# Performance work log

Measured on AMD Instinct MI355X. Metric: run time of the kernel, lower is better.

Reference implementation:

```python
import jax, jax.numpy as jnp
import numpy as np

K = 32
TEMPERATURE = 0.1
RTOL, ATOL = 1e-5, 1e-5


def _embed(x, W1, b1, W2, b2, W3, b3):
    h = jax.nn.gelu(x @ W1.T + b1, approximate=False)
    h = jax.nn.gelu(h @ W2.T + b2, approximate=False)
    return jax.nn.sigmoid(h @ W3.T + b3)


def setup_inputs() -> dict:
    key = jax.random.key(0)
    ks = jax.random.split(key, 9)
    Q, N, D_IN, D_E = 256, 16384, 256, 64
    s = lambda fan_in: 1.0 / np.sqrt(fan_in)
    return {
        "x": jax.random.normal(ks[0], (Q, D_IN), jnp.float32),
        "support_x": jax.random.normal(ks[1], (N, D_IN), jnp.float32),
        "support_labels": jax.random.uniform(ks[2], (N, 1), jnp.float32),
        "W1": jax.random.normal(ks[3], (D_E, D_IN), jnp.float32) * s(D_IN),
        "b1": jax.random.normal(ks[4], (D_E,), jnp.float32) * s(D_IN),
        "W2": jax.random.normal(ks[5], (D_E, D_E), jnp.float32) * s(D_E),
        "b2": jax.random.normal(ks[6], (D_E,), jnp.float32) * s(D_E),
        "W3": jax.random.normal(ks[7], (D_E, D_E), jnp.float32) * s(D_E),
        "b3": jax.random.normal(ks[8], (D_E,), jnp.float32) * s(D_E),
    }


def reference(x, support_x, support_labels, W1, b1, W2, b2, W3, b3):
    # query embeddings [Q, D]; support embeddings [N, D] (set_support is no_grad)
    q = _embed(x, W1, b1, W2, b2, W3, b3)
    s = jax.lax.stop_gradient(_embed(support_x, W1, b1, W2, b2, W3, b3))
    # torch.cdist p=2 via expanded squared distances
    d2 = (jnp.sum(q * q, -1)[:, None] + jnp.sum(s * s, -1)[None, :]
          - 2.0 * (q @ s.T))
    dist = jnp.sqrt(jnp.maximum(d2, 0.0))  # [Q, N]
    # isclose mask: |q - s| <= atol + rtol*|s|, all over feature dim
    close = jnp.abs(q[:, None, :] - s[None, :, :]) <= (ATOL + RTOL * jnp.abs(s)[None, :, :])
    mask = jnp.all(close, axis=-1)  # [Q, N]
    dist = jnp.where(mask, jnp.inf, dist)
    # top-k smallest distances
    neg_top, idx = jax.lax.top_k(-dist, K)  # [Q, K]
    topd = -neg_top
    neighbor_labels = support_labels[idx].squeeze(-1)  # [Q, K]
    weights = jax.nn.softmax(-topd / TEMPERATURE, axis=1)
    return jnp.sum(weights * neighbor_labels, axis=1)  # [Q]
```

## Files before the change

kernel.cpp:

```cpp
#include <hip/hip_runtime.h>
#include <math.h>

#define D_IN   256
#define D_E    64
#define N_SUP  16384
#define NQ     256
#define KSEL   32
#define RTOLC  1e-5f
#define ATOLC  1e-5f
#define INV_T  10.0f

#define CHUNK  1024
#define NCH    16
#define QG     8
#define NQG    32

typedef unsigned long long ull;

__device__ __forceinline__ float gelu_exact(float x) {
    return 0.5f * x * (1.0f + erff(x * 0.70710678118654752440f));
}

__global__ __launch_bounds__(256) void prep_w(
    const float* __restrict__ W1, const float* __restrict__ W2,
    const float* __restrict__ W3,
    float* __restrict__ W1T, float* __restrict__ W2T, float* __restrict__ W3T)
{
    const int t = blockIdx.x * 256 + threadIdx.x;
    const int stride = gridDim.x * 256;
    for (int o = t; o < D_E * D_IN; o += stride) {
        int f = o >> 8, k = o & 255;
        W1T[k * D_E + f] = W1[o];
    }
    for (int o = t; o < D_E * D_E; o += stride) {
        int f = o >> 6, k = o & 63;
        W2T[k * D_E + f] = W2[o];
        W3T[k * D_E + f] = W3[o];
    }
}

__global__ __launch_bounds__(512, 6) void embed_kernel(
    const float* __restrict__ sx, const float* __restrict__ x,
    const float* __restrict__ W1T, const float* __restrict__ b1,
    const float* __restrict__ W2T, const float* __restrict__ b2,
    const float* __restrict__ W3T, const float* __restrict__ b3,
    float* __restrict__ s_emb, float* __restrict__ s_norm,
    float* __restrict__ q_emb, float* __restrict__ q_norm)
{
    __shared__ float xc[64][65];
    __shared__ float hA[64][65];
    __shared__ float hB[64][65];
    __shared__ float nsum[64][9];

    const int tid  = threadIdx.x;
    const int lane = tid & 63;
    const int wv   = tid >> 6;
    const int f0   = __builtin_amdgcn_readfirstlane(wv * 8);
    const bool isq = blockIdx.x >= (N_SUP / 64);
    const float* src = isq ? (x + (size_t)(blockIdx.x - N_SUP / 64) * 64 * D_IN)
                           : (sx + (size_t)blockIdx.x * 64 * D_IN);

    float acc[8];
    #pragma unroll
    for (int i = 0; i < 8; ++i) acc[i] = b1[f0 + i];

    for (int kc = 0; kc < 4; ++kc) {
        __syncthreads();
        #pragma unroll
        for (int i = 0; i < 2; ++i) {
            int g   = i * 512 + tid;
            int row = g >> 4;
            int c4  = g & 15;
            float4 v = *reinterpret_cast<const float4*>(
                src + (size_t)row * D_IN + kc * 64 + c4 * 4);
            xc[c4 * 4 + 0][row] = v.x; xc[c4 * 4 + 1][row] = v.y;
            xc[c4 * 4 + 2][row] = v.z; xc[c4 * 4 + 3][row] = v.w;
        }
        __syncthreads();
        const float* wbase = W1T + (size_t)(kc * 64) * D_E + f0;
        #pragma unroll 8
        for (int k = 0; k < 64; ++k) {
            float xk = xc[k][lane];
            const float* wk = wbase + k * D_E;
            #pragma unroll
            for (int f = 0; f < 8; ++f) acc[f] = fmaf(wk[f], xk, acc[f]);
        }
    }
    #pragma unroll
    for (int i = 0; i < 8; ++i) hA[f0 + i][lane] = gelu_exact(acc[i]);
    __syncthreads();

    float a2[8];
    #pragma unroll
    for (int i = 0; i < 8; ++i) a2[i] = b2[f0 + i];
    #pragma unroll 8
    for (int k = 0; k < D_E; ++k) {
        float hk = hA[k][lane];
        const float* wk = W2T + k * D_E + f0;
        #pragma unroll
        for (int f = 0; f < 8; ++f) a2[f] = fmaf(wk[f], hk, a2[f]);
    }
    #pragma unroll
    for (int i = 0; i < 8; ++i) hB[f0 + i][lane] = gelu_exact(a2[i]);
    __syncthreads();

    float a3[8];
    #pragma unroll
    for (int i = 0; i < 8; ++i) a3[i] = b3[f0 + i];
    #pragma unroll 8
    for (int k = 0; k < D_E; ++k) {
        float hk = hB[k][lane];
        const float* wk = W3T + k * D_E + f0;
        #pragma unroll
        for (int f = 0; f < 8; ++f) a3[f] = fmaf(wk[f], hk, a3[f]);
    }
    float e[8];
    float np = 0.0f;
    #pragma unroll
    for (int i = 0; i < 8; ++i) {
        e[i] = 1.0f / (1.0f + expf(-a3[i]));
        np = fmaf(e[i], e[i], np);
    }

    const int rowl = isq ? (blockIdx.x - N_SUP / 64) * 64 + lane
                         : blockIdx.x * 64 + lane;
    float* E   = isq ? q_emb  : s_emb;
    float* Nrm = isq ? q_norm : s_norm;
    float* erow = E + (size_t)rowl * D_E + f0;
    *reinterpret_cast<float4*>(erow)     = make_float4(e[0], e[1], e[2], e[3]);
    *reinterpret_cast<float4*>(erow + 4) = make_float4(e[4], e[5], e[6], e[7]);

    nsum[lane][wv] = np;
    __syncthreads();
    if (wv == 0) {
        float s = 0.0f;
        #pragma unroll
        for (int w = 0; w < 8; ++w) s += nsum[lane][w];
        Nrm[rowl] = s;
    }
}

__global__ __launch_bounds__(512, 4) void knn_phaseA(
    const float* __restrict__ s_emb, const float* __restrict__ s_norm,
    const float* __restrict__ q_emb, const float* __restrict__ q_norm,
    const float* __restrict__ labels, ull* __restrict__ cand)
{
    __shared__ float tile[64 * 68];
    __shared__ float d2l[QG][CHUNK];
    __shared__ ull   win_l[QG][KSEL];

    const int tid  = threadIdx.x;
    const int lane = tid & 63;
    const int wid  = tid >> 6;
    const int qg   = blockIdx.x >> 4;
    const int sc   = blockIdx.x & 15;
    const int qiu  = __builtin_amdgcn_readfirstlane(qg * QG + wid);

    const float* q0 = q_emb + (size_t)qiu * D_E;
    const float  qn = q_norm[qiu];

    for (int s = 0; s < 16; ++s) {
        __syncthreads();
        #pragma unroll
        for (int i = 0; i < 2; ++i) {
            int g   = i * 512 + tid;
            int row = g >> 4, c4 = g & 15;
            float4 v = *reinterpret_cast<const float4*>(
                s_emb + (size_t)(sc * CHUNK + s * 64 + row) * D_E + c4 * 4);
            *reinterpret_cast<float4*>(&tile[row * 68 + c4 * 4]) = v;
        }
        __syncthreads();

        const float* tr = &tile[lane * 68];
        float a = 0.0f;
        #pragma unroll
        for (int c = 0; c < 16; ++c) {
            float4 sv = *reinterpret_cast<const float4*>(tr + c * 4);
            a = fmaf(q0[c * 4 + 0], sv.x, a);
            a = fmaf(q0[c * 4 + 1], sv.y, a);
            a = fmaf(q0[c * 4 + 2], sv.z, a);
            a = fmaf(q0[c * 4 + 3], sv.w, a);
        }
        const int grow = sc * CHUNK + s * 64 + lane;
        float d2 = fmaxf(qn + s_norm[grow] - 2.0f * a, 0.0f);
        if (d2 < 1e-3f) {
            bool close = true;
            for (int k = 0; k < D_E; ++k) {
                float sv = tr[k];
                close = close && (fabsf(q0[k] - sv) <= (ATOLC + RTOLC * fabsf(sv)));
            }
            if (close) d2 = INFINITY;
        }
        d2l[wid][s * 64 + lane] = d2;
    }

    ull sk[16];
    #pragma unroll
    for (int j = 0; j < 16; ++j) {
        float d2 = d2l[wid][j * 64 + lane];
        sk[j] = ((ull)__float_as_uint(d2) << 10) | (unsigned)(j * 64 + lane);
    }

    #pragma unroll
    for (int k = 2; k <= 16; k <<= 1) {
        #pragma unroll
        for (int j = k >> 1; j > 0; j >>= 1) {
            #pragma unroll
            for (int i = 0; i < 16; ++i) {
                int ixj = i ^ j;
                if (ixj > i) {
                    if ((i & k) == 0) {
                        ull a_ = sk[i], b_ = sk[ixj];
                        bool c_ = b_ < a_;
                        sk[i] = c_ ? b_ : a_; sk[ixj] = c_ ? a_ : b_;
                    } else {
                        ull a_ = sk[i], b_ = sk[ixj];
                        bool c_ = a_ < b_;
                        sk[i] = c_ ? b_ : a_; sk[ixj] = c_ ? a_ : b_;
                    }
                }
            }
        }
    }

    ull lkey = sk[0];
    for (int it = 0; it < KSEL; ++it) {
        ull m = lkey;
        #pragma unroll
        for (int off = 1; off < 64; off <<= 1) {
            ull o = __shfl_xor(m, off);
            m = o < m ? o : m;
        }
        if (lane == it) win_l[wid][it] = m;
        if (lkey == m) {
            #pragma unroll
            for (int j = 0; j < 15; ++j) sk[j] = sk[j + 1];
            sk[15] = ~0ull;
            lkey = sk[0];
        }
    }

    if (lane < KSEL) {
        ull m = win_l[wid][lane];
        unsigned gidx = (unsigned)(sc * CHUNK) + (unsigned)(m & 1023u);
        float lab = labels[gidx];
        ull* dst = cand + ((size_t)qiu * NCH + sc) * KSEL;
        dst[lane] = ((ull)(unsigned)(m >> 10) << 32) | (ull)__float_as_uint(lab);
    }
}

__global__ __launch_bounds__(256) void knn_phaseB(
    const ull* __restrict__ cand, float* __restrict__ out)
{
    const int lane = threadIdx.x & 63;
    const int wid  = threadIdx.x >> 6;
    const int q    = blockIdx.x * 4 + wid;

    const bool act = lane < NCH;
    const ull* lst = cand + ((size_t)q * NCH + (lane & 15)) * KSEL;
    int ptr = 0;
    ull cur = act ? lst[0] : ~0ull;

    float d0 = 0.0f, sw = 0.0f, sl = 0.0f;
    for (int it = 0; it < KSEL; ++it) {
        unsigned mv = (unsigned)(cur >> 32);
        unsigned ml = (unsigned)cur;
        #pragma unroll
        for (int off = 1; off < 16; off <<= 1) {
            unsigned ov = __shfl_xor(mv, off);
            unsigned ol = __shfl_xor(ml, off);
            bool take = (ov < mv) || (ov == mv && (lane & off));
            mv = take ? ov : mv;
            ml = take ? ol : ml;
        }
        ull b = __ballot(act && (unsigned)(cur >> 32) == mv);
        int wl = (int)(__ffsll((long long)b) - 1);
        if (lane == wl) {
            ++ptr;
            cur = (ptr < KSEL) ? lst[ptr] : ~0ull;
        }
        if (lane == 0) {
            float d = sqrtf(__uint_as_float(mv));
            if (it == 0) d0 = d;
            float w = expf((d0 - d) * INV_T);
            sw += w;
            sl += w * __uint_as_float(ml);
        }
    }
    if (lane == 0) out[q] = sl / sw;
}

extern "C" void kernel_launch(void* const* d_in, const int* in_sizes, int n_in,
                              void* d_out, int out_size, void* d_ws, size_t ws_size,
                              hipStream_t stream) {
    const float* x      = (const float*)d_in[0];
    const float* sx     = (const float*)d_in[1];
    const float* labels = (const float*)d_in[2];
    const float* W1     = (const float*)d_in[3];
    const float* b1     = (const float*)d_in[4];
    const float* W2     = (const float*)d_in[5];
    const float* b2     = (const float*)d_in[6];
    const float* W3     = (const float*)d_in[7];
    const float* b3     = (const float*)d_in[8];
    float* out = (float*)d_out;

    float* ws     = (float*)d_ws;
    float* s_emb  = ws;
    float* s_norm = s_emb + N_SUP * D_E;
    float* q_emb  = s_norm + N_SUP;
    float* q_norm = q_emb + NQ * D_E;
    float* W1T    = q_norm + NQ;
    float* W2T    = W1T + D_IN * D_E;
    float* W3T    = W2T + D_E * D_E;
    ull*   cand   = (ull*)(W3T + D_E * D_E);

    prep_w<<<32, 256, 0, stream>>>(W1, W2, W3, W1T, W2T, W3T);
    embed_kernel<<<(N_SUP + NQ) / 64, 512, 0, stream>>>(
        sx, x, W1T, b1, W2T, b2, W3T, b3, s_emb, s_norm, q_emb, q_norm);
    knn_phaseA<<<NQG * NCH, 512, 0, stream>>>(s_emb, s_norm, q_emb, q_norm,
                                              labels, cand);
    knn_phaseB<<<NQ / 4, 256, 0, stream>>>(cand, out);
}
```

Before: 101.6 us.

## Restructure embed and kNN kernels with shared-memory weight tiles and double buffering

The embed kernel drops the separate weight-transpose kernel and now stages W1/W2/W3 through shared memory in double-buffered tiles, using 16-row blocks with 256 threads where each thread computes 4 features. The kNN phase A caches query embeddings in LDS, double-buffers support tiles, and remaps lanes so each wave covers 8 queries by 8 rows. Its top-k merge now reduces 32-bit distance keys with a ballot-based tie-break in place of 64-bit shuffles. These changes target global weight reads, one kernel launch, and shuffle cost, at the price of more blocks and lower declared occupancy in phase A.

New measurement: 111.5 us. +9.7%, slower.

```diff
diff --git a/kernel.cpp b/kernel.cpp
--- a/kernel.cpp
+++ b/kernel.cpp
@@ -14,6 +14,7 @@
 #define NCH    16
 #define QG     8
 #define NQG    32
+#define EROWS  16
 
 typedef unsigned long long ull;
 
@@ -21,132 +22,148 @@
     return 0.5f * x * (1.0f + erff(x * 0.70710678118654752440f));
 }
 
-__global__ __launch_bounds__(256) void prep_w(
-    const float* __restrict__ W1, const float* __restrict__ W2,
-    const float* __restrict__ W3,
-    float* __restrict__ W1T, float* __restrict__ W2T, float* __restrict__ W3T)
-{
-    const int t = blockIdx.x * 256 + threadIdx.x;
-    const int stride = gridDim.x * 256;
-    for (int o = t; o < D_E * D_IN; o += stride) {
-        int f = o >> 8, k = o & 255;
-        W1T[k * D_E + f] = W1[o];
-    }
-    for (int o = t; o < D_E * D_E; o += stride) {
-        int f = o >> 6, k = o & 63;
-        W2T[k * D_E + f] = W2[o];
-        W3T[k * D_E + f] = W3[o];
-    }
-}
-
-__global__ __launch_bounds__(512, 6) void embed_kernel(
+__global__ __launch_bounds__(256, 4) void embed_kernel(
     const float* __restrict__ sx, const float* __restrict__ x,
-    const float* __restrict__ W1T, const float* __restrict__ b1,
-    const float* __restrict__ W2T, const float* __restrict__ b2,
-    const float* __restrict__ W3T, const float* __restrict__ b3,
+    const float* __restrict__ W1, const float* __restrict__ b1,
+    const float* __restrict__ W2, const float* __restrict__ b2,
+    const float* __restrict__ W3, const float* __restrict__ b3,
     float* __restrict__ s_emb, float* __restrict__ s_norm,
     float* __restrict__ q_emb, float* __restrict__ q_norm)
 {
-    __shared__ float xc[64][65];
-    __shared__ float hA[64][65];
-    __shared__ float hB[64][65];
-    __shared__ float nsum[64][9];
-
-    const int tid  = threadIdx.x;
-    const int lane = tid & 63;
-    const int wv   = tid >> 6;
-    const int f0   = __builtin_amdgcn_readfirstlane(wv * 8);
-    const bool isq = blockIdx.x >= (N_SUP / 64);
-    const float* src = isq ? (x + (size_t)(blockIdx.x - N_SUP / 64) * 64 * D_IN)
-                           : (sx + (size_t)blockIdx.x * 64 * D_IN);
-
-    float acc[8];
-    #pragma unroll
-    for (int i = 0; i < 8; ++i) acc[i] = b1[f0 + i];
-
+    __shared__ float xc[2][64][17];
+    __shared__ float wc[2][64][68];
+    __shared__ float hA[64][17];
+    __shared__ float nsq[16][17];
+
+    const int tid = threadIdx.x;
+    const int r   = tid & 15;
+    const int fg4 = (tid >> 4) * 4;
+    const bool isq = blockIdx.x >= (N_SUP / EROWS);
+    const float* src = isq ? (x + (size_t)(blockIdx.x - N_SUP / EROWS) * EROWS * D_IN)
+                           : (sx + (size_t)blockIdx.x * EROWS * D_IN);
+
+    #define STAGE_X(kc_, b_)                                                   \
+        {                                                                      \
+            int row_ = tid >> 4, c4_ = tid & 15;                               \
+            float4 v_ = *reinterpret_cast<const float4*>(                      \
+                src + (size_t)row_ * D_IN + (kc_) * 64 + c4_ * 4);             \
+            xc[b_][c4_ * 4 + 0][row_] = v_.x;                                  \
+            xc[b_][c4_ * 4 + 1][row_] = v_.y;                                  \
+            xc[b_][c4_ * 4 + 2][row_] = v_.z;                                  \
+            xc[b_][c4_ * 4 + 3][row_] = v_.w;                                  \
+        }
+    #define STAGE_W1(kc_, b_)                                                  \
+        {                                                                      \
+            _Pragma("unroll")                                                  \
+            for (int i_ = 0; i_ < 4; ++i_) {                                   \
+                int g_ = i_ * 256 + tid;                                       \
+                int f_ = g_ >> 4, c4_ = g_ & 15;                               \
+                float4 w_ = *reinterpret_cast<const float4*>(                  \
+                    W1 + (size_t)f_ * D_IN + (kc_) * 64 + c4_ * 4);            \
+                wc[b_][c4_ * 4 + 0][f_] = w_.x;                                \
+                wc[b_][c4_ * 4 + 1][f_] = w_.y;                                \
+                wc[b_][c4_ * 4 + 2][f_] = w_.z;                                \
+                wc[b_][c4_ * 4 + 3][f_] = w_.w;                                \
+            }                                                                  \
+        }
+
+    STAGE_X(0, 0);
+    STAGE_W1(0, 0);
+    __syncthreads();
+
+    float4 bv1 = *reinterpret_cast<const float4*>(b1 + fg4);
+    float acc[4] = {bv1.x, bv1.y, bv1.z, bv1.w};
     for (int kc = 0; kc < 4; ++kc) {
-        __syncthreads();
-        #pragma unroll
-        for (int i = 0; i < 2; ++i) {
-            int g   = i * 512 + tid;
-            int row = g >> 4;
-            int c4  = g & 15;
-            float4 v = *reinterpret_cast<const float4*>(
-                src + (size_t)row * D_IN + kc * 64 + c4 * 4);
-            xc[c4 * 4 + 0][row] = v.x; xc[c4 * 4 + 1][row] = v.y;
-            xc[c4 * 4 + 2][row] = v.z; xc[c4 * 4 + 3][row] = v.w;
-        }
-        __syncthreads();
-        const float* wbase = W1T + (size_t)(kc * 64) * D_E + f0;
+        const int b = kc & 1;
+        if (kc < 3) { STAGE_X(kc + 1, b ^ 1); STAGE_W1(kc + 1, b ^ 1); }
         #pragma unroll 8
         for (int k = 0; k < 64; ++k) {
-            float xk = xc[k][lane];
-            const float* wk = wbase + k * D_E;
-            #pragma unroll
-            for (int f = 0; f < 8; ++f) acc[f] = fmaf(wk[f], xk, acc[f]);
-        }
-    }
-    #pragma unroll
-    for (int i = 0; i < 8; ++i) hA[f0 + i][lane] = gelu_exact(acc[i]);
-    __syncthreads();
-
-    float a2[8];
-    #pragma unroll
-    for (int i = 0; i < 8; ++i) a2[i] = b2[f0 + i];
+            float xk = xc[b][k][r];
+            float4 wv = *reinterpret_cast<const float4*>(&wc[b][k][fg4]);
+            acc[0] = fmaf(wv.x, xk, acc[0]);
+            acc[1] = fmaf(wv.y, xk, acc[1]);
+            acc[2] = fmaf(wv.z, xk, acc[2]);
+            acc[3] = fmaf(wv.w, xk, acc[3]);
+        }
+        __syncthreads();
+    }
+    #pragma unroll
+    for (int i = 0; i < 4; ++i) hA[fg4 + i][r] = gelu_exact(acc[i]);
+    #pragma unroll
+    for (int i = 0; i < 4; ++i) {
+        int g = i * 256 + tid;
+        int f = g >> 4, c4 = g & 15;
+        float4 w2 = *reinterpret_cast<const float4*>(W2 + (size_t)f * D_E + c4 * 4);
+        wc[0][c4 * 4 + 0][f] = w2.x; wc[0][c4 * 4 + 1][f] = w2.y;
+        wc[0][c4 * 4 + 2][f] = w2.z; wc[0][c4 * 4 + 3][f] = w2.w;
+        float4 w3 = *reinterpret_cast<const float4*>(W3 + (size_t)f * D_E + c4 * 4);
+        wc[1][c4 * 4 + 0][f] = w3.x; wc[1][c4 * 4 + 1][f] = w3.y;
+        wc[1][c4 * 4 + 2][f] = w3.z; wc[1][c4 * 4 + 3][f] = w3.w;
+    }
+    __syncthreads();
+
+    float4 bv2 = *reinterpret_cast<const float4*>(b2 + fg4);
+    float a2[4] = {bv2.x, bv2.y, bv2.z, bv2.w};
     #pragma unroll 8
     for (int k = 0; k < D_E; ++k) {
-        float hk = hA[k][lane];
-        const float* wk = W2T + k * D_E + f0;
-        #pragma unroll
-        for (int f = 0; f < 8; ++f) a2[f] = fmaf(wk[f], hk, a2[f]);
-    }
-    #pragma unroll
-    for (int i = 0; i < 8; ++i) hB[f0 + i][lane] = gelu_exact(a2[i]);
-    __syncthreads();
-
-    float a3[8];
-    #pragma unroll
-    for (int i = 0; i < 8; ++i) a3[i] = b3[f0 + i];
+        float hk = hA[k][r];
+        float4 wv = *reinterpret_cast<const float4*>(&wc[0][k][fg4]);
+        a2[0] = fmaf(wv.x, hk, a2[0]);
+        a2[1] = fmaf(wv.y, hk, a2[1]);
+        a2[2] = fmaf(wv.z, hk, a2[2]);
+        a2[3] = fmaf(wv.w, hk, a2[3]);
+    }
+    #pragma unroll
+    for (int i = 0; i < 4; ++i) xc[0][fg4 + i][r] = gelu_exact(a2[i]);
+    __syncthreads();
+
+    float4 bv3 = *reinterpret_cast<const float4*>(b3 + fg4);
+    float a3[4] = {bv3.x, bv3.y, bv3.z, bv3.w};
     #pragma unroll 8
     for (int k = 0; k < D_E; ++k) {
-        float hk = hB[k][lane];
-        const float* wk = W3T + k * D_E + f0;
-        #pragma unroll
-        for (int f = 0; f < 8; ++f) a3[f] = fmaf(wk[f], hk, a3[f]);
-    }
-    float e[8];
+        float hk = xc[0][k][r];
+        float4 wv = *reinterpret_cast<const float4*>(&wc[1][k][fg4]);
+        a3[0] = fmaf(wv.x, hk, a3[0]);
+        a3[1] = fmaf(wv.y, hk, a3[1]);
+        a3[2] = fmaf(wv.z, hk, a3[2]);
+        a3[3] = fmaf(wv.w, hk, a3[3]);
+    }
+    float e[4];
     float np = 0.0f;
     #pragma unroll
-    for (int i = 0; i < 8; ++i) {
+    for (int i = 0; i < 4; ++i) {
         e[i] = 1.0f / (1.0f + expf(-a3[i]));
         np = fmaf(e[i], e[i], np);
     }
 
-    const int rowl = isq ? (blockIdx.x - N_SUP / 64) * 64 + lane
-                         : blockIdx.x * 64 + lane;
+    const int rowg = (isq ? (blockIdx.x - N_SUP / EROWS) * EROWS : blockIdx.x * EROWS) + r;
     float* E   = isq ? q_emb  : s_emb;
     float* Nrm = isq ? q_norm : s_norm;
-    float* erow = E + (size_t)rowl * D_E + f0;
-    *reinterpret_cast<float4*>(erow)     = make_float4(e[0], e[1], e[2], e[3]);
-    *reinterpret_cast<float4*>(erow + 4) = make_float4(e[4], e[5], e[6], e[7]);
-
-    nsum[lane][wv] = np;
-    __syncthreads();
-    if (wv == 0) {
-        float s = 0.0f;
-        #pragma unroll
-        for (int w = 0; w < 8; ++w) s += nsum[lane][w];
-        Nrm[rowl] = s;
-    }
-}
-
-__global__ __launch_bounds__(512, 4) void knn_phaseA(
+    *reinterpret_cast<float4*>(E + (size_t)rowg * D_E + fg4) =
+        make_float4(e[0], e[1], e[2], e[3]);
+
+    nsq[r][fg4 >> 2] = np;
+    __syncthreads();
+    if (tid < EROWS) {
+        float s = nsq[tid][0];
+        #pragma unroll
+        for (int g = 1; g < 16; ++g) s += nsq[tid][g];
+        const int rg = (isq ? (blockIdx.x - N_SUP / EROWS) * EROWS : blockIdx.x * EROWS) + tid;
+        Nrm[rg] = s;
+    }
+    #undef STAGE_X
+    #undef STAGE_W1
+}
+
+__global__ __launch_bounds__(512, 2) void knn_phaseA(
     const float* __restrict__ s_emb, const float* __restrict__ s_norm,
     const float* __restrict__ q_emb, const float* __restrict__ q_norm,
     const float* __restrict__ labels, ull* __restrict__ cand)
 {
-    __shared__ float tile[64 * 68];
-    __shared__ float d2l[QG][CHUNK];
+    __shared__ float tile[2][64 * 68];
+    __shared__ float d2l[QG][1032];
+    __shared__ float qs[QG][68];
+    __shared__ float qn_l[QG];
     __shared__ ull   win_l[QG][KSEL];
 
     const int tid  = threadIdx.x;
@@ -154,44 +171,64 @@
     const int wid  = tid >> 6;
     const int qg   = blockIdx.x >> 4;
     const int sc   = blockIdx.x & 15;
-    const int qiu  = __builtin_amdgcn_readfirstlane(qg * QG + wid);
-
-    const float* q0 = q_emb + (size_t)qiu * D_E;
-    const float  qn = q_norm[qiu];
-
-    for (int s = 0; s < 16; ++s) {
-        __syncthreads();
+
+    {
+        int q = tid >> 6, c = tid & 63;
+        qs[q][c] = q_emb[(size_t)(qg * QG + q) * D_E + c];
+        if (tid < QG) qn_l[tid] = q_norm[qg * QG + tid];
         #pragma unroll
         for (int i = 0; i < 2; ++i) {
-            int g   = i * 512 + tid;
+            int g = i * 512 + tid;
             int row = g >> 4, c4 = g & 15;
             float4 v = *reinterpret_cast<const float4*>(
-                s_emb + (size_t)(sc * CHUNK + s * 64 + row) * D_E + c4 * 4);
-            *reinterpret_cast<float4*>(&tile[row * 68 + c4 * 4]) = v;
-        }
-        __syncthreads();
-
-        const float* tr = &tile[lane * 68];
+                s_emb + (size_t)(sc * CHUNK + row) * D_E + c4 * 4);
+            *reinterpret_cast<float4*>(&tile[0][row * 68 + c4 * 4]) = v;
+        }
+    }
+    __syncthreads();
+
+    const int ql   = lane >> 3;
+    const int rsub = lane & 7;
+    const int rloc = wid * 8 + rsub;
+    const float qn = qn_l[ql];
+
+    for (int s = 0; s < 16; ++s) {
+        const int b = s & 1;
+        if (s < 15) {
+            #pragma unroll
+            for (int i = 0; i < 2; ++i) {
+                int g = i * 512 + tid;
+                int row = g >> 4, c4 = g & 15;
+                float4 v = *reinterpret_cast<const float4*>(
+                    s_emb + (size_t)(sc * CHUNK + (s + 1) * 64 + row) * D_E + c4 * 4);
+                *reinterpret_cast<float4*>(&tile[b ^ 1][row * 68 + c4 * 4]) = v;
+            }
+        }
+
+        const float* tr = &tile[b][rloc * 68];
+        const float* qp = &qs[ql][0];
         float a = 0.0f;
         #pragma unroll
         for (int c = 0; c < 16; ++c) {
             float4 sv = *reinterpret_cast<const float4*>(tr + c * 4);
-            a = fmaf(q0[c * 4 + 0], sv.x, a);
-            a = fmaf(q0[c * 4 + 1], sv.y, a);
-            a = fmaf(q0[c * 4 + 2], sv.z, a);
-            a = fmaf(q0[c * 4 + 3], sv.w, a);
-        }
-        const int grow = sc * CHUNK + s * 64 + lane;
+            float4 qv = *reinterpret_cast<const float4*>(qp + c * 4);
+            a = fmaf(qv.x, sv.x, a);
+            a = fmaf(qv.y, sv.y, a);
+            a = fmaf(qv.z, sv.z, a);
+            a = fmaf(qv.w, sv.w, a);
+        }
+        const int grow = sc * CHUNK + s * 64 + rloc;
         float d2 = fmaxf(qn + s_norm[grow] - 2.0f * a, 0.0f);
         if (d2 < 1e-3f) {
             bool close = true;
             for (int k = 0; k < D_E; ++k) {
-                float sv = tr[k];
-                close = close && (fabsf(q0[k] - sv) <= (ATOLC + RTOLC * fabsf(sv)));
+                float svk = tr[k];
+                close = close && (fabsf(qs[ql][k] - svk) <= (ATOLC + RTOLC * fabsf(svk)));
             }
             if (close) d2 = INFINITY;
         }
-        d2l[wid][s * 64 + lane] = d2;
+        d2l[ql][s * 64 + rloc] = d2;
+        __syncthreads();
     }
 
     ull sk[16];
@@ -224,19 +261,33 @@
     }
 
     ull lkey = sk[0];
+    unsigned lv = (unsigned)(lkey >> 10);
     for (int it = 0; it < KSEL; ++it) {
-        ull m = lkey;
+        unsigned m = lv;
         #pragma unroll
         for (int off = 1; off < 64; off <<= 1) {
-            ull o = __shfl_xor(m, off);
+            unsigned o = __shfl_xor(m, off);
             m = o < m ? o : m;
         }
-        if (lane == it) win_l[wid][it] = m;
-        if (lkey == m) {
+        ull tb = __ballot(lv == m);
+        if (__popcll(tb) > 1) {
+            unsigned rr = (lv == m) ? (unsigned)(lkey & 1023u) : 0xffffffffu;
+            unsigned rm = rr;
+            #pragma unroll
+            for (int off = 1; off < 64; off <<= 1) {
+                unsigned o = __shfl_xor(rm, off);
+                rm = o < rm ? o : rm;
+            }
+            tb = __ballot(rr == rm);
+        }
+        const int wl = (int)(__ffsll((long long)tb) - 1);
+        if (lane == wl) {
+            win_l[wid][it] = lkey;
             #pragma unroll
             for (int j = 0; j < 15; ++j) sk[j] = sk[j + 1];
             sk[15] = ~0ull;
             lkey = sk[0];
+            lv = (unsigned)(lkey >> 10);
         }
     }
 
@@ -244,7 +295,7 @@
         ull m = win_l[wid][lane];
         unsigned gidx = (unsigned)(sc * CHUNK) + (unsigned)(m & 1023u);
         float lab = labels[gidx];
-        ull* dst = cand + ((size_t)qiu * NCH + sc) * KSEL;
+        ull* dst = cand + ((size_t)(qg * QG + wid) * NCH + sc) * KSEL;
         dst[lane] = ((ull)(unsigned)(m >> 10) << 32) | (ull)__float_as_uint(lab);
     }
 }
@@ -309,14 +360,10 @@
     float* s_norm = s_emb + N_SUP * D_E;
     float* q_emb  = s_norm + N_SUP;
     float* q_norm = q_emb + NQ * D_E;
-    float* W1T    = q_norm + NQ;
-    float* W2T    = W1T + D_IN * D_E;
-    float* W3T    = W2T + D_E * D_E;
-    ull*   cand   = (ull*)(W3T + D_E * D_E);
-
-    prep_w<<<32, 256, 0, stream>>>(W1, W2, W3, W1T, W2T, W3T);
-    embed_kernel<<<(N_SUP + NQ) / 64, 512, 0, stream>>>(
-        sx, x, W1T, b1, W2T, b2, W3T, b3, s_emb, s_norm, q_emb, q_norm);
+    ull*   cand   = (ull*)(q_norm + NQ);
+
+    embed_kernel<<<(N_SUP + NQ) / EROWS, 256, 0, stream>>>(
+        sx, x, W1, b1, W2, b2, W3, b3, s_emb, s_norm, q_emb, q_norm);
     knn_phaseA<<<NQG * NCH, 512, 0, stream>>>(s_emb, s_norm, q_emb, q_norm,
                                               labels, cand);
     knn_phaseB<<<NQ / 4, 256, 0, stream>>>(cand, out);
```

## Restructure embedding MLP and double-buffer kNN distance tiles with finer chunks

Applied to the files above, without the earlier changes.

The embedding kernel now gives each thread one output feature and keeps its packed float4 weights in registers. Input rows are read straight from global memory with wave-uniform addresses instead of being staged through transposed shared-memory tiles, and the row norm is computed with a wave shuffle reduction. The kNN phase A uses 512-element chunks and 32 chunks, which doubles the block count. It double-buffers support tiles with register prefetch and keeps distances in registers rather than a shared array, so the bitonic sort shrinks to 8 elements. The wave argmin now works on 32-bit keys with a tie-break pass, and phase B merges 32 candidate lists. The risks are higher register pressure and a larger candidate merge.

After: 228.2 us. 125% more time.

```diff
diff --git a/kernel.cpp b/kernel.cpp
--- a/kernel.cpp
+++ b/kernel.cpp
@@ -10,8 +10,8 @@
 #define ATOLC  1e-5f
 #define INV_T  10.0f
 
-#define CHUNK  1024
-#define NCH    16
+#define CHUNK  512
+#define NCH    32
 #define QG     8
 #define NQG    32
 
@@ -24,154 +24,172 @@
 __global__ __launch_bounds__(256) void prep_w(
     const float* __restrict__ W1, const float* __restrict__ W2,
     const float* __restrict__ W3,
-    float* __restrict__ W1T, float* __restrict__ W2T, float* __restrict__ W3T)
+    float4* __restrict__ W1P, float4* __restrict__ W2P, float4* __restrict__ W3P)
 {
     const int t = blockIdx.x * 256 + threadIdx.x;
-    const int stride = gridDim.x * 256;
-    for (int o = t; o < D_E * D_IN; o += stride) {
-        int f = o >> 8, k = o & 255;
-        W1T[k * D_E + f] = W1[o];
-    }
-    for (int o = t; o < D_E * D_E; o += stride) {
-        int f = o >> 6, k = o & 63;
-        W2T[k * D_E + f] = W2[o];
-        W3T[k * D_E + f] = W3[o];
-    }
-}
-
-__global__ __launch_bounds__(512, 6) void embed_kernel(
+    if (t < 64 * 64) {
+        int k4 = t >> 6, f = t & 63;
+        const float* w = W1 + (size_t)f * D_IN + 4 * k4;
+        W1P[t] = make_float4(w[0], w[1], w[2], w[3]);
+    }
+    if (t < 16 * 64) {
+        int k4 = t >> 6, f = t & 63;
+        const float* w2 = W2 + (size_t)f * D_E + 4 * k4;
+        W2P[t] = make_float4(w2[0], w2[1], w2[2], w2[3]);
+        const float* w3 = W3 + (size_t)f * D_E + 4 * k4;
+        W3P[t] = make_float4(w3[0], w3[1], w3[2], w3[3]);
+    }
+}
+
+__global__ __launch_bounds__(256) void embed_kernel(
     const float* __restrict__ sx, const float* __restrict__ x,
-    const float* __restrict__ W1T, const float* __restrict__ b1,
-    const float* __restrict__ W2T, const float* __restrict__ b2,
-    const float* __restrict__ W3T, const float* __restrict__ b3,
+    const float4* __restrict__ W1P, const float* __restrict__ b1,
+    const float4* __restrict__ W2P, const float* __restrict__ b2,
+    const float4* __restrict__ W3P, const float* __restrict__ b3,
     float* __restrict__ s_emb, float* __restrict__ s_norm,
     float* __restrict__ q_emb, float* __restrict__ q_norm)
 {
-    __shared__ float xc[64][65];
-    __shared__ float hA[64][65];
-    __shared__ float hB[64][65];
-    __shared__ float nsum[64][9];
-
-    const int tid  = threadIdx.x;
-    const int lane = tid & 63;
-    const int wv   = tid >> 6;
-    const int f0   = __builtin_amdgcn_readfirstlane(wv * 8);
-    const bool isq = blockIdx.x >= (N_SUP / 64);
-    const float* src = isq ? (x + (size_t)(blockIdx.x - N_SUP / 64) * 64 * D_IN)
-                           : (sx + (size_t)blockIdx.x * 64 * D_IN);
-
+    __shared__ float hl[32][68];
+
+    const int tid = threadIdx.x;
+    const int f   = tid & 63;
+    const int wv  = tid >> 6;
+    const int r0  = __builtin_amdgcn_readfirstlane(wv * 8);
+    const bool isq = blockIdx.x >= (N_SUP / 32);
+    const int  rowbase = isq ? (int)(blockIdx.x - N_SUP / 32) * 32
+                             : (int)blockIdx.x * 32;
+    const float* src = (isq ? x : sx) + (size_t)rowbase * D_IN;
+
+    const float b1v = b1[f];
     float acc[8];
     #pragma unroll
-    for (int i = 0; i < 8; ++i) acc[i] = b1[f0 + i];
-
+    for (int r = 0; r < 8; ++r) acc[r] = b1v;
+
+    #pragma unroll
     for (int kc = 0; kc < 4; ++kc) {
-        __syncthreads();
-        #pragma unroll
-        for (int i = 0; i < 2; ++i) {
-            int g   = i * 512 + tid;
-            int row = g >> 4;
-            int c4  = g & 15;
-            float4 v = *reinterpret_cast<const float4*>(
-                src + (size_t)row * D_IN + kc * 64 + c4 * 4);
-            xc[c4 * 4 + 0][row] = v.x; xc[c4 * 4 + 1][row] = v.y;
-            xc[c4 * 4 + 2][row] = v.z; xc[c4 * 4 + 3][row] = v.w;
-        }
-        __syncthreads();
-        const float* wbase = W1T + (size_t)(kc * 64) * D_E + f0;
-        #pragma unroll 8
-        for (int k = 0; k < 64; ++k) {
-            float xk = xc[k][lane];
-            const float* wk = wbase + k * D_E;
-            #pragma unroll
-            for (int f = 0; f < 8; ++f) acc[f] = fmaf(wk[f], xk, acc[f]);
-        }
-    }
-    #pragma unroll
-    for (int i = 0; i < 8; ++i) hA[f0 + i][lane] = gelu_exact(acc[i]);
-    __syncthreads();
-
-    float a2[8];
-    #pragma unroll
-    for (int i = 0; i < 8; ++i) a2[i] = b2[f0 + i];
-    #pragma unroll 8
-    for (int k = 0; k < D_E; ++k) {
-        float hk = hA[k][lane];
-        const float* wk = W2T + k * D_E + f0;
-        #pragma unroll
-        for (int f = 0; f < 8; ++f) a2[f] = fmaf(wk[f], hk, a2[f]);
-    }
-    #pragma unroll
-    for (int i = 0; i < 8; ++i) hB[f0 + i][lane] = gelu_exact(a2[i]);
-    __syncthreads();
-
-    float a3[8];
-    #pragma unroll
-    for (int i = 0; i < 8; ++i) a3[i] = b3[f0 + i];
-    #pragma unroll 8
-    for (int k = 0; k < D_E; ++k) {
-        float hk = hB[k][lane];
-        const float* wk = W3T + k * D_E + f0;
-        #pragma unroll
-        for (int f = 0; f < 8; ++f) a3[f] = fmaf(wk[f], hk, a3[f]);
-    }
-    float e[8];
-    float np = 0.0f;
-    #pragma unroll
-    for (int i = 0; i < 8; ++i) {
-        e[i] = 1.0f / (1.0f + expf(-a3[i]));
-        np = fmaf(e[i], e[i], np);
-    }
-
-    const int rowl = isq ? (blockIdx.x - N_SUP / 64) * 64 + lane
-                         : blockIdx.x * 64 + lane;
-    float* E   = isq ? q_emb  : s_emb;
-    float* Nrm = isq ? q_norm : s_norm;
-    float* erow = E + (size_t)rowl * D_E + f0;
-    *reinterpret_cast<float4*>(erow)     = make_float4(e[0], e[1], e[2], e[3]);
-    *reinterpret_cast<float4*>(erow + 4) = make_float4(e[4], e[5], e[6], e[7]);
-
-    nsum[lane][wv] = np;
-    __syncthreads();
-    if (wv == 0) {
-        float s = 0.0f;
-        #pragma unroll
-        for (int w = 0; w < 8; ++w) s += nsum[lane][w];
-        Nrm[rowl] = s;
-    }
-}
-
-__global__ __launch_bounds__(512, 4) void knn_phaseA(
+        float4 wreg[16];
+        #pragma unroll
+        for (int j = 0; j < 16; ++j)
+            wreg[j] = W1P[(kc * 16 + j) * 64 + f];
+        #pragma unroll
+        for (int j = 0; j < 16; ++j) {
+            #pragma unroll
+            for (int r = 0; r < 8; ++r) {
+                const float* xp = src + (size_t)(r0 + r) * D_IN + kc * 64 + j * 4;
+                acc[r] = fmaf(wreg[j].x, xp[0], acc[r]);
+                acc[r] = fmaf(wreg[j].y, xp[1], acc[r]);
+                acc[r] = fmaf(wreg[j].z, xp[2], acc[r]);
+                acc[r] = fmaf(wreg[j].w, xp[3], acc[r]);
+            }
+        }
+    }
+    #pragma unroll
+    for (int r = 0; r < 8; ++r) hl[r0 + r][f] = gelu_exact(acc[r]);
+
+    {
+        float4 wreg[16];
+        #pragma unroll
+        for (int j = 0; j < 16; ++j) wreg[j] = W2P[j * 64 + f];
+        const float b2v = b2[f];
+        float a2[8];
+        #pragma unroll
+        for (int r = 0; r < 8; ++r) a2[r] = b2v;
+        #pragma unroll
+        for (int j = 0; j < 16; ++j) {
+            #pragma unroll
+            for (int r = 0; r < 8; ++r) {
+                float4 hv = *reinterpret_cast<const float4*>(&hl[r0 + r][4 * j]);
+                a2[r] = fmaf(wreg[j].x, hv.x, a2[r]);
+                a2[r] = fmaf(wreg[j].y, hv.y, a2[r]);
+                a2[r] = fmaf(wreg[j].z, hv.z, a2[r]);
+                a2[r] = fmaf(wreg[j].w, hv.w, a2[r]);
+            }
+        }
+        #pragma unroll
+        for (int r = 0; r < 8; ++r) acc[r] = gelu_exact(a2[r]);
+    }
+    #pragma unroll
+    for (int r = 0; r < 8; ++r) hl[r0 + r][f] = acc[r];
+
+    {
+        float4 wreg[16];
+        #pragma unroll
+        for (int j = 0; j < 16; ++j) wreg[j] = W3P[j * 64 + f];
+        const float b3v = b3[f];
+        float a3[8];
+        #pragma unroll
+        for (int r = 0; r < 8; ++r) a3[r] = b3v;
+        #pragma unroll
+        for (int j = 0; j < 16; ++j) {
+            #pragma unroll
+            for (int r = 0; r < 8; ++r) {
+                float4 hv = *reinterpret_cast<const float4*>(&hl[r0 + r][4 * j]);
+                a3[r] = fmaf(wreg[j].x, hv.x, a3[r]);
+                a3[r] = fmaf(wreg[j].y, hv.y, a3[r]);
+                a3[r] = fmaf(wreg[j].z, hv.z, a3[r]);
+                a3[r] = fmaf(wreg[j].w, hv.w, a3[r]);
+            }
+        }
+        float* E   = isq ? q_emb  : s_emb;
+        float* Nrm = isq ? q_norm : s_norm;
+        float nr[8];
+        #pragma unroll
+        for (int r = 0; r < 8; ++r) {
+            float e = 1.0f / (1.0f + expf(-a3[r]));
+            E[(size_t)(rowbase + r0 + r) * D_E + f] = e;
+            nr[r] = e * e;
+        }
+        #pragma unroll
+        for (int off = 1; off < 64; off <<= 1) {
+            #pragma unroll
+            for (int r = 0; r < 8; ++r) nr[r] += __shfl_xor(nr[r], off);
+        }
+        if (f == 0) {
+            #pragma unroll
+            for (int r = 0; r < 8; ++r) Nrm[rowbase + r0 + r] = nr[r];
+        }
+    }
+}
+
+__global__ __launch_bounds__(512, 2) void knn_phaseA(
     const float* __restrict__ s_emb, const float* __restrict__ s_norm,
     const float* __restrict__ q_emb, const float* __restrict__ q_norm,
     const float* __restrict__ labels, ull* __restrict__ cand)
 {
-    __shared__ float tile[64 * 68];
-    __shared__ float d2l[QG][CHUNK];
+    __shared__ float tile[2][64 * 68];
     __shared__ ull   win_l[QG][KSEL];
 
     const int tid  = threadIdx.x;
     const int lane = tid & 63;
     const int wid  = tid >> 6;
-    const int qg   = blockIdx.x >> 4;
-    const int sc   = blockIdx.x & 15;
+    const int qg   = blockIdx.x >> 5;
+    const int sc   = blockIdx.x & 31;
     const int qiu  = __builtin_amdgcn_readfirstlane(qg * QG + wid);
-
     const float* q0 = q_emb + (size_t)qiu * D_E;
     const float  qn = q_norm[qiu];
 
-    for (int s = 0; s < 16; ++s) {
-        __syncthreads();
-        #pragma unroll
-        for (int i = 0; i < 2; ++i) {
-            int g   = i * 512 + tid;
-            int row = g >> 4, c4 = g & 15;
-            float4 v = *reinterpret_cast<const float4*>(
-                s_emb + (size_t)(sc * CHUNK + s * 64 + row) * D_E + c4 * 4);
-            *reinterpret_cast<float4*>(&tile[row * 68 + c4 * 4]) = v;
-        }
-        __syncthreads();
-
-        const float* tr = &tile[lane * 68];
+    #pragma unroll
+    for (int i = 0; i < 2; ++i) {
+        int g = i * 512 + tid;
+        int row = g >> 4, c4 = g & 15;
+        float4 v = *reinterpret_cast<const float4*>(
+            s_emb + (size_t)(sc * CHUNK + row) * D_E + c4 * 4);
+        *reinterpret_cast<float4*>(&tile[0][row * 68 + c4 * 4]) = v;
+    }
+    __syncthreads();
+
+    float d2s[8];
+    #pragma unroll
+    for (int s = 0; s < 8; ++s) {
+        const int b = s & 1;
+        float4 p0, p1;
+        if (s < 7) {
+            p0 = *reinterpret_cast<const float4*>(
+                s_emb + (size_t)(sc * CHUNK + (s + 1) * 64 + (tid >> 4)) * D_E + (tid & 15) * 4);
+            p1 = *reinterpret_cast<const float4*>(
+                s_emb + (size_t)(sc * CHUNK + (s + 1) * 64 + ((512 + tid) >> 4)) * D_E + (tid & 15) * 4);
+        }
+        const float* tr = &tile[b][lane * 68];
         float a = 0.0f;
         #pragma unroll
         for (int c = 0; c < 16; ++c) {
@@ -186,38 +204,36 @@
         if (d2 < 1e-3f) {
             bool close = true;
             for (int k = 0; k < D_E; ++k) {
-                float sv = tr[k];
-                close = close && (fabsf(q0[k] - sv) <= (ATOLC + RTOLC * fabsf(sv)));
+                float svk = tr[k];
+                close = close && (fabsf(q0[k] - svk) <= (ATOLC + RTOLC * fabsf(svk)));
             }
             if (close) d2 = INFINITY;
         }
-        d2l[wid][s * 64 + lane] = d2;
-    }
-
-    ull sk[16];
-    #pragma unroll
-    for (int j = 0; j < 16; ++j) {
-        float d2 = d2l[wid][j * 64 + lane];
-        sk[j] = ((ull)__float_as_uint(d2) << 10) | (unsigned)(j * 64 + lane);
-    }
-
-    #pragma unroll
-    for (int k = 2; k <= 16; k <<= 1) {
+        d2s[s] = d2;
+        if (s < 7) {
+            *reinterpret_cast<float4*>(&tile[b ^ 1][(tid >> 4) * 68 + (tid & 15) * 4]) = p0;
+            *reinterpret_cast<float4*>(&tile[b ^ 1][((512 + tid) >> 4) * 68 + (tid & 15) * 4]) = p1;
+        }
+        __syncthreads();
+    }
+
+    ull sk[8];
+    #pragma unroll
+    for (int j = 0; j < 8; ++j)
+        sk[j] = ((ull)__float_as_uint(d2s[j]) << 9) | (unsigned)(j * 64 + lane);
+
+    #pragma unroll
+    for (int k = 2; k <= 8; k <<= 1) {
         #pragma unroll
         for (int j = k >> 1; j > 0; j >>= 1) {
             #pragma unroll
-            for (int i = 0; i < 16; ++i) {
+            for (int i = 0; i < 8; ++i) {
                 int ixj = i ^ j;
                 if (ixj > i) {
-                    if ((i & k) == 0) {
-                        ull a_ = sk[i], b_ = sk[ixj];
-                        bool c_ = b_ < a_;
-                        sk[i] = c_ ? b_ : a_; sk[ixj] = c_ ? a_ : b_;
-                    } else {
-                        ull a_ = sk[i], b_ = sk[ixj];
-                        bool c_ = a_ < b_;
-                        sk[i] = c_ ? b_ : a_; sk[ixj] = c_ ? a_ : b_;
-                    }
+                    ull a_ = sk[i], b_ = sk[ixj];
+                    bool up = (i & k) == 0;
+                    bool c_ = up ? (b_ < a_) : (a_ < b_);
+                    sk[i] = c_ ? b_ : a_; sk[ixj] = c_ ? a_ : b_;
                 }
             }
         }
@@ -225,27 +241,40 @@
 
     ull lkey = sk[0];
     for (int it = 0; it < KSEL; ++it) {
-        ull m = lkey;
+        unsigned lv = (unsigned)(lkey >> 9);
+        unsigned m = lv;
         #pragma unroll
         for (int off = 1; off < 64; off <<= 1) {
-            ull o = __shfl_xor(m, off);
+            unsigned o = __shfl_xor(m, off);
             m = o < m ? o : m;
         }
-        if (lane == it) win_l[wid][it] = m;
-        if (lkey == m) {
-            #pragma unroll
-            for (int j = 0; j < 15; ++j) sk[j] = sk[j + 1];
-            sk[15] = ~0ull;
+        ull tb = __ballot(lv == m);
+        if (__popcll(tb) > 1) {
+            unsigned rr = (lv == m) ? (unsigned)(lkey & 511u) : 0xffffffffu;
+            unsigned rm = rr;
+            #pragma unroll
+            for (int off = 1; off < 64; off <<= 1) {
+                unsigned o = __shfl_xor(rm, off);
+                rm = o < rm ? o : rm;
+            }
+            tb = __ballot(rr == rm);
+        }
+        const int wl = (int)(__ffsll((long long)tb) - 1);
+        if (lane == wl) {
+            win_l[wid][it] = lkey;
+            #pragma unroll
+            for (int j = 0; j < 7; ++j) sk[j] = sk[j + 1];
+            sk[7] = ~0ull;
             lkey = sk[0];
         }
     }
 
     if (lane < KSEL) {
         ull m = win_l[wid][lane];
-        unsigned gidx = (unsigned)(sc * CHUNK) + (unsigned)(m & 1023u);
+        unsigned gidx = (unsigned)(sc * CHUNK) + (unsigned)(m & 511u);
         float lab = labels[gidx];
         ull* dst = cand + ((size_t)qiu * NCH + sc) * KSEL;
-        dst[lane] = ((ull)(unsigned)(m >> 10) << 32) | (ull)__float_as_uint(lab);
+        dst[lane] = ((ull)(unsigned)(m >> 9) << 32) | (ull)__float_as_uint(lab);
     }
 }
 
@@ -257,7 +286,7 @@
     const int q    = blockIdx.x * 4 + wid;
 
     const bool act = lane < NCH;
-    const ull* lst = cand + ((size_t)q * NCH + (lane & 15)) * KSEL;
+    const ull* lst = cand + ((size_t)q * NCH + (lane & 31)) * KSEL;
     int ptr = 0;
     ull cur = act ? lst[0] : ~0ull;
 
@@ -266,15 +295,15 @@
         unsigned mv = (unsigned)(cur >> 32);
         unsigned ml = (unsigned)cur;
         #pragma unroll
-        for (int off = 1; off < 16; off <<= 1) {
+        for (int off = 1; off < 32; off <<= 1) {
             unsigned ov = __shfl_xor(mv, off);
             unsigned ol = __shfl_xor(ml, off);
             bool take = (ov < mv) || (ov == mv && (lane & off));
             mv = take ? ov : mv;
             ml = take ? ol : ml;
         }
-        ull b = __ballot(act && (unsigned)(cur >> 32) == mv);
-        int wl = (int)(__ffsll((long long)b) - 1);
+        ull bl = __ballot(act && (unsigned)(cur >> 32) == mv);
+        int wl = (int)(__ffsll((long long)bl) - 1);
         if (lane == wl) {
             ++ptr;
             cur = (ptr < KSEL) ? lst[ptr] : ~0ull;
@@ -306,17 +335,17 @@
 
     float* ws     = (float*)d_ws;
     float* s_emb  = ws;
-    float* s_norm = s_emb + N_SUP * D_E;
+    float* s_norm = s_emb + (size_t)N_SUP * D_E;
     float* q_emb  = s_norm + N_SUP;
-    float* q_norm = q_emb + NQ * D_E;
-    float* W1T    = q_norm + NQ;
-    float* W2T    = W1T + D_IN * D_E;
-    float* W3T    = W2T + D_E * D_E;
-    ull*   cand   = (ull*)(W3T + D_E * D_E);
-
-    prep_w<<<32, 256, 0, stream>>>(W1, W2, W3, W1T, W2T, W3T);
-    embed_kernel<<<(N_SUP + NQ) / 64, 512, 0, stream>>>(
-        sx, x, W1T, b1, W2T, b2, W3T, b3, s_emb, s_norm, q_emb, q_norm);
+    float* q_norm = q_emb + (size_t)NQ * D_E;
+    ull*   cand   = (ull*)(q_norm + NQ);
+    float4* W1P   = (float4*)(cand + (size_t)NQ * NCH * KSEL);
+    float4* W2P   = W1P + 64 * 64;
+    float4* W3P   = W2P + 16 * 64;
+
+    prep_w<<<16, 256, 0, stream>>>(W1, W2, W3, W1P, W2P, W3P);
+    embed_kernel<<<(N_SUP + NQ) / 32, 256, 0, stream>>>(
+        sx, x, W1P, b1, W2P, b2, W3P, b3, s_emb, s_norm, q_emb, q_norm);
     knn_phaseA<<<NQG * NCH, 512, 0, stream>>>(s_emb, s_norm, q_emb, q_norm,
                                               labels, cand);
     knn_phaseB<<<NQ / 4, 256, 0, stream>>>(cand, out);
```
